# Kernel optimization log

Hardware: AMD Instinct MI355X
Metric: run time of the kernel (lower is better)

## Reference

```python
import jax, jax.numpy as jnp
import numpy as np

# QLSTMClassifier (quantum mode): Embedding -> QLSTM (4 quantum gate layers per step) -> Linear -> log_softmax.
# NOTE: QLSTM.forward unbinds dim 0 (batch) and cats each x:(seq,emb) with hx:(batch,hid),
# which requires batch == seq_len. We honor that with S = batch = seq_len.
S = 256   # batch == seq_len
E = 1024  # embedding_dim
H = 10    # hidden_dim == n_qubits (required by f*cx elementwise product)
V = 50257 # vocab_size
T = 50    # tagset_size


def setup_inputs() -> dict:
    key = jax.random.key(0)
    ks = jax.random.split(key, 6)
    sentence = jax.random.randint(ks[0], (S, S), 0, V)                                   # (batch, seq)
    emb_table = jax.random.normal(ks[1], (V, E), jnp.float32) * 0.02                      # nn.Embedding weight
    Wg = jax.random.normal(ks[2], (4, E + H, H), jnp.float32) * (1.0 / np.sqrt(E + H))    # forget/input/update/output linears
    bg = jnp.zeros((4, H), jnp.float32)
    theta = jax.random.normal(ks[3], (4, H), jnp.float32)                                 # trainable RX angles per gate
    W_out = jax.random.normal(ks[4], (H, T), jnp.float32) * (1.0 / np.sqrt(H))            # hidden2tag
    b_out = jnp.zeros((T,), jnp.float32)
    return dict(sentence=sentence, emb_table=emb_table, Wg=Wg, bg=bg,
                theta=theta, W_out=W_out, b_out=b_out)


def _qlayer(z, th):
    # Exact closed form of the QLayer circuit on n wires starting from |0...0>:
    #   RX(z_w) then RX(th_w) on wire w  ==> RX(a_w) with a_w = z_w + th_w (product state),
    #   then CNOT ring: CNOT(0,1), CNOT(1,2), ..., CNOT(n-2,n-1), CNOT(n-1,0),
    # Heisenberg-picture pullback of Z_w through the CNOT ring gives
    #   M_0 = Z_1 Z_2 ... Z_{n-1},   M_w = Z_0 Z_1 ... Z_w  (w >= 1),
    # and on the product state <Z_j> = cos(a_j), so expectations factorize:
    #   out_0 = prod_{j>=1} cos(a_j),  out_w = prod_{j<=w} cos(a_j).
    c = jnp.cos(z + th)                                   # (B, H)
    cum = jnp.cumprod(c, axis=-1)                         # prefix products
    tail = jnp.prod(c[:, 1:], axis=-1, keepdims=True)     # wire-0 observable
    return jnp.concatenate([tail, cum[:, 1:]], axis=-1)   # (B, H)


def reference(sentence, emb_table, Wg, bg, theta, W_out, b_out):
    embeds = emb_table[sentence]                          # (S, S, E); scan axis = dim 0 (unbind dim)
    h0 = jnp.zeros((embeds.shape[0], theta.shape[1]), embeds.dtype)

    def step(carry, x):                                   # x: (S, E)
        hx, cx = carry
        comb = jnp.concatenate([x, hx], axis=-1)          # (S, E+H)
        z = jnp.einsum('bi,gio->gbo', comb, Wg) + bg[:, None, :]  # (4, S, H)
        f = jax.nn.sigmoid(_qlayer(z[0], theta[0]))
        i = jax.nn.sigmoid(_qlayer(z[1], theta[1]))
        g = jnp.tanh(_qlayer(z[2], theta[2]))
        o = jax.nn.sigmoid(_qlayer(z[3], theta[3]))
        cx = f * cx + i * g
        hx = o * jnp.tanh(cx)
        return (hx, cx), hx

    _, outs = jax.lax.scan(step, (h0, h0), embeds)        # (S, S, H)
    logits = outs @ W_out + b_out                         # (S, S, T)
    return jax.nn.log_softmax(logits, axis=2)
```

## Files before the change

### kernel.cpp

```cpp
#include <hip/hip_runtime.h>
#include <hip/hip_bf16.h>


#define E_DIM 1024
#define H_DIM 10
#define NC 40
#define EHS 10340

typedef __attribute__((ext_vector_type(8))) short bf16x8;
typedef __attribute__((ext_vector_type(4))) float f32x4;

__device__ __forceinline__ unsigned short f2bf(float f) {
    unsigned u = __float_as_uint(f);
    unsigned r = u + 0x7FFFu + ((u >> 16) & 1u);
    return (unsigned short)(r >> 16);
}

__global__ __launch_bounds__(256) void k_wt(const float* __restrict__ Wg,
                                            unsigned short* __restrict__ Bfg) {
    int i = blockIdx.x * 256 + threadIdx.x;
    if (i >= 6144) return;
    int lane = i & 63, nt = (i >> 6) % 3, c = i / 192;
    int kg = lane >> 4, n = lane & 15;
    int nc = nt * 16 + n;
    unsigned short v[8];
#pragma unroll
    for (int j = 0; j < 8; ++j) {
        int k = c * 32 + kg * 8 + j;
        float w = 0.0f;
        if (nc < NC) {
            int g = nc / H_DIM, h = nc % H_DIM;
            w = Wg[g * EHS + k * H_DIM + h];
        }
        v[j] = f2bf(w);
    }
    bf16x8* dst = (bf16x8*)(Bfg + (size_t)i * 8);
    bf16x8 pk;
#pragma unroll
    for (int j = 0; j < 8; ++j) pk[j] = (short)v[j];
    *dst = pk;
}

__global__ __launch_bounds__(256, 4) void k_gemm(const int* __restrict__ idx,
                                                 const float* __restrict__ emb,
                                                 const unsigned short* __restrict__ Bfg,
                                                 float* __restrict__ zs) {
    const int tid = threadIdx.x;
    const int wave = tid >> 6, lane = tid & 63;
    const int R0 = (blockIdx.x * 4 + wave) * 16;
    const int m = lane & 15, q = lane >> 4;

    const int token = idx[R0 + m];
    const float* arow = emb + (size_t)token * E_DIM + q * 8;

    f32x4 acc0 = {0.f, 0.f, 0.f, 0.f}, acc1 = acc0, acc2 = acc0;

#pragma unroll 2
    for (int c = 0; c < 32; ++c) {
        float4 a0 = *(const float4*)(arow + c * 32);
        float4 a1 = *(const float4*)(arow + c * 32 + 4);
        bf16x8 b0 = *(const bf16x8*)(Bfg + ((size_t)(c * 3 + 0) * 64 + lane) * 8);
        bf16x8 b1 = *(const bf16x8*)(Bfg + ((size_t)(c * 3 + 1) * 64 + lane) * 8);
        bf16x8 b2 = *(const bf16x8*)(Bfg + ((size_t)(c * 3 + 2) * 64 + lane) * 8);
        bf16x8 af;
        af[0] = (short)f2bf(a0.x); af[1] = (short)f2bf(a0.y);
        af[2] = (short)f2bf(a0.z); af[3] = (short)f2bf(a0.w);
        af[4] = (short)f2bf(a1.x); af[5] = (short)f2bf(a1.y);
        af[6] = (short)f2bf(a1.z); af[7] = (short)f2bf(a1.w);
        acc0 = __builtin_amdgcn_mfma_f32_16x16x32_bf16(af, b0, acc0, 0, 0, 0);
        acc1 = __builtin_amdgcn_mfma_f32_16x16x32_bf16(af, b1, acc1, 0, 0, 0);
        acc2 = __builtin_amdgcn_mfma_f32_16x16x32_bf16(af, b2, acc2, 0, 0, 0);
    }

    const int t = R0 >> 8;
    const int bbase = (R0 & 255) + q * 4;
#pragma unroll
    for (int i = 0; i < 4; ++i) {
        int b = bbase + i;
        size_t o = ((size_t)b * 256 + t) * NC;
        zs[o + m] = acc0[i];
        zs[o + 16 + m] = acc1[i];
        if (m < 8) zs[o + 32 + m] = acc2[i];
    }
}

template <int CTRL>
__device__ __forceinline__ float dpp1(float x) {
    return __int_as_float(__builtin_amdgcn_update_dpp(
        __float_as_int(1.0f), __float_as_int(x), CTRL, 0xF, 0xF, false));
}
#define ROW_SHR(n) (0x110 + (n))
#define ROW_SHL(n) (0x100 + (n))

__device__ __forceinline__ float rdlane(float v, int l) {
    return __int_as_float(__builtin_amdgcn_readlane(__float_as_int(v), l));
}

__global__ __launch_bounds__(128) void k_rnn(const float* __restrict__ zs,
                                             const float* __restrict__ Wg,
                                             const float* __restrict__ bg,
                                             const float* __restrict__ theta,
                                             float* __restrict__ outs) {
    __shared__ float zbuf[2][640];
    const int tid = threadIdx.x;
    const int b = blockIdx.x;

    if (tid >= 64) {
        const int p = tid - 64;
        const float* src = zs + (size_t)b * 256 * NC;
#pragma unroll
        for (int k = 0; k < 10; ++k) zbuf[0][p + k * 64] = src[p + k * 64];
        __syncthreads();
        for (int blk = 0; blk < 16; ++blk) {
            if (blk + 1 < 16) {
                const float* s2 = src + (blk + 1) * 640;
                float v[10];
#pragma unroll
                for (int k = 0; k < 10; ++k) v[k] = s2[p + k * 64];
#pragma unroll
                for (int k = 0; k < 10; ++k) zbuf[(blk + 1) & 1][p + k * 64] = v[k];
            }
            __syncthreads();
        }
    } else {
        const int lane = tid;
        const int r = lane >> 4;
        const int h = lane & 15;
        const int hc = (h < 10) ? h : 9;
        const int cidx = r * 10 + hc;

        float Wh[10];
#pragma unroll
        for (int j = 0; j < 10; ++j) Wh[j] = Wg[r * EHS + (E_DIM + j) * H_DIM + hc];
        const float bias = bg[cidx] + theta[cidx];

        const float kk = (r == 2) ? 2.0f : -1.0f;
        const float aa = (r == 2) ? 1.0f : 0.0f;
        const float bb = (r == 2) ? -2.0f : 1.0f;

        float cx = 0.0f, hx = 0.0f;
        __syncthreads();

        for (int blk = 0; blk < 16; ++blk) {
            const float* zb = zbuf[blk & 1];
            float zv = zb[cidx];
#pragma unroll 4
            for (int s = 0; s < 16; ++s) {
                float znext = zb[((s < 15) ? (s + 1) * 40 : s * 40) + cidx];

                float hv0 = rdlane(hx, 0), hv1 = rdlane(hx, 1), hv2 = rdlane(hx, 2),
                      hv3 = rdlane(hx, 3), hv4 = rdlane(hx, 4), hv5 = rdlane(hx, 5),
                      hv6 = rdlane(hx, 6), hv7 = rdlane(hx, 7), hv8 = rdlane(hx, 8),
                      hv9 = rdlane(hx, 9);
                float d0 = fmaf(hv0, Wh[0], fmaf(hv2, Wh[2],
                           fmaf(hv4, Wh[4], fmaf(hv6, Wh[6], hv8 * Wh[8]))));
                float d1 = fmaf(hv1, Wh[1], fmaf(hv3, Wh[3],
                           fmaf(hv5, Wh[5], fmaf(hv7, Wh[7], hv9 * Wh[9]))));
                float z = (zv + bias) + (d0 + d1);

                float cc = __builtin_amdgcn_cosf(z * 0.15915494309189535f);

                float pp = cc;
                pp *= dpp1<ROW_SHR(1)>(pp);
                pp *= dpp1<ROW_SHR(2)>(pp);
                pp *= dpp1<ROW_SHR(4)>(pp);
                pp *= dpp1<ROW_SHR(8)>(pp);
                float ss = (h < 10) ? cc : 1.0f;
                ss *= dpp1<ROW_SHL(1)>(ss);
                ss *= dpp1<ROW_SHL(2)>(ss);
                ss *= dpp1<ROW_SHL(4)>(ss);
                ss *= dpp1<ROW_SHL(8)>(ss);
                float tl = dpp1<ROW_SHL(1)>(ss);
                float qv = (h == 0) ? tl : pp;

                float e = __expf(kk * qv);
                float act = fmaf(bb, __builtin_amdgcn_rcpf(1.0f + e), aa);

                float fv = __shfl(act, h);
                float iv = __shfl(act, 16 + h);
                float gv = __shfl(act, 32 + h);
                float ov = __shfl(act, 48 + h);

                cx = fmaf(fv, cx, iv * gv);
                float e2 = __expf(2.0f * cx);
                float th = fmaf(-2.0f, __builtin_amdgcn_rcpf(1.0f + e2), 1.0f);
                hx = ov * th;

                int t = blk * 16 + s;
                if (lane < 10) outs[((size_t)t * 256 + b) * H_DIM + lane] = hx;
                zv = znext;
            }
            __syncthreads();
        }
    }
}

__global__ __launch_bounds__(256) void k_head(const float* __restrict__ outs,
                                              const float* __restrict__ Wo,
                                              const float* __restrict__ bo,
                                              float* __restrict__ out) {
    const size_t row = blockIdx.x * 256 + threadIdx.x;
    float hx[10];
#pragma unroll
    for (int i = 0; i < 5; ++i) {
        float2 v = *(const float2*)&outs[row * H_DIM + 2 * i];
        hx[2 * i] = v.x; hx[2 * i + 1] = v.y;
    }
    float lg[50];
#pragma unroll
    for (int cI = 0; cI < 50; ++cI) {
        float l = bo[cI];
#pragma unroll
        for (int j = 0; j < 10; ++j) l = fmaf(hx[j], Wo[j * 50 + cI], l);
        lg[cI] = l;
    }
    float m = lg[0];
#pragma unroll
    for (int cI = 1; cI < 50; ++cI) m = fmaxf(m, lg[cI]);
    float sum = 0.0f;
#pragma unroll
    for (int cI = 0; cI < 50; ++cI) sum += __expf(lg[cI] - m);
    float lse = m + __logf(sum);
#pragma unroll
    for (int i = 0; i < 25; ++i) {
        float2 v = {lg[2 * i] - lse, lg[2 * i + 1] - lse};
        *(float2*)&out[row * 50 + 2 * i] = v;
    }
}

extern "C" void kernel_launch(void* const* d_in, const int* in_sizes, int n_in,
                              void* d_out, int out_size, void* d_ws, size_t ws_size,
                              hipStream_t stream) {
    const int*   sentence = (const int*)d_in[0];
    const float* emb      = (const float*)d_in[1];
    const float* Wg       = (const float*)d_in[2];
    const float* bg       = (const float*)d_in[3];
    const float* theta    = (const float*)d_in[4];
    const float* Wo       = (const float*)d_in[5];
    const float* bo       = (const float*)d_in[6];
    float* out = (float*)d_out;

    float* ws = (float*)d_ws;
    unsigned short* Bfg = (unsigned short*)ws;
    float* zs   = ws + 24576;
    float* outs = zs + (size_t)256 * 256 * NC;

    k_wt<<<24, 256, 0, stream>>>(Wg, Bfg);
    k_gemm<<<1024, 256, 0, stream>>>(sentence, emb, Bfg, zs);
    k_rnn<<<256, 128, 0, stream>>>(zs, Wg, bg, theta, outs);
    k_head<<<256, 256, 0, stream>>>(outs, Wo, bo, out);
}
```

Measured before the change: 381.5 us.

## Stage embedding rows into LDS via async global_load_lds with double buffering

The gather GEMM no longer reads embedding rows straight from global memory into registers. Each wave now streams its 16 gathered rows into a per-wave double-buffered LDS region with global_load_lds, in 256-float chunks, and hand-placed vmcnt waits let the next chunk load while MFMAs run on the current one. B fragments for eight k-steps are also loaded into registers ahead of use. The cost is 130KB of LDS per block, which forces one block per CU and lowers occupancy, and correctness now depends on the hard-coded vmcnt counts.

Result: no change. 385.6 us (+1.1%).

```diff
diff --git a/kernel.cpp b/kernel.cpp
--- a/kernel.cpp
+++ b/kernel.cpp
@@ -41,35 +41,82 @@
     *dst = pk;
 }
 
-__global__ __launch_bounds__(256, 4) void k_gemm(const int* __restrict__ idx,
+#define CH_F 256
+#define ROWB 1040
+#define WBUF (16 * ROWB)
+#define WAVE_LDS (2 * WBUF)
+
+typedef const __attribute__((address_space(1))) void* gas1_t;
+typedef __attribute__((address_space(3))) void* las3_t;
+
+__device__ __forceinline__ void gload_lds16(const void* g, void* l) {
+    __builtin_amdgcn_global_load_lds((gas1_t)(unsigned long long)g,
+                                     (las3_t)(unsigned)(unsigned long long)l,
+                                     16, 0, 0);
+}
+
+__global__ __launch_bounds__(256, 1) void k_gemm(const int* __restrict__ idx,
                                                  const float* __restrict__ emb,
                                                  const unsigned short* __restrict__ Bfg,
                                                  float* __restrict__ zs) {
+    __shared__ char smem[4 * WAVE_LDS];
     const int tid = threadIdx.x;
     const int wave = tid >> 6, lane = tid & 63;
-    const int R0 = (blockIdx.x * 4 + wave) * 16;
+    const int R0 = blockIdx.x * 64 + wave * 16;
     const int m = lane & 15, q = lane >> 4;
 
-    const int token = idx[R0 + m];
-    const float* arow = emb + (size_t)token * E_DIM + q * 8;
+    char* mybuf = smem + wave * WAVE_LDS;
+
+    const int tok = idx[R0 + m];
+    const float* grow[16];
+#pragma unroll
+    for (int j = 0; j < 16; ++j) {
+        int tj = __builtin_amdgcn_readlane(tok, j);
+        grow[j] = emb + (size_t)tj * E_DIM;
+    }
 
     f32x4 acc0 = {0.f, 0.f, 0.f, 0.f}, acc1 = acc0, acc2 = acc0;
 
-#pragma unroll 2
-    for (int c = 0; c < 32; ++c) {
-        float4 a0 = *(const float4*)(arow + c * 32);
-        float4 a1 = *(const float4*)(arow + c * 32 + 4);
-        bf16x8 b0 = *(const bf16x8*)(Bfg + ((size_t)(c * 3 + 0) * 64 + lane) * 8);
-        bf16x8 b1 = *(const bf16x8*)(Bfg + ((size_t)(c * 3 + 1) * 64 + lane) * 8);
-        bf16x8 b2 = *(const bf16x8*)(Bfg + ((size_t)(c * 3 + 2) * 64 + lane) * 8);
-        bf16x8 af;
-        af[0] = (short)f2bf(a0.x); af[1] = (short)f2bf(a0.y);
-        af[2] = (short)f2bf(a0.z); af[3] = (short)f2bf(a0.w);
-        af[4] = (short)f2bf(a1.x); af[5] = (short)f2bf(a1.y);
-        af[6] = (short)f2bf(a1.z); af[7] = (short)f2bf(a1.w);
-        acc0 = __builtin_amdgcn_mfma_f32_16x16x32_bf16(af, b0, acc0, 0, 0, 0);
-        acc1 = __builtin_amdgcn_mfma_f32_16x16x32_bf16(af, b1, acc1, 0, 0, 0);
-        acc2 = __builtin_amdgcn_mfma_f32_16x16x32_bf16(af, b2, acc2, 0, 0, 0);
+#pragma unroll
+    for (int j = 0; j < 16; ++j)
+        gload_lds16(grow[j] + lane * 4, mybuf + j * ROWB);
+
+#pragma unroll
+    for (int cc = 0; cc < 4; ++cc) {
+        bf16x8 Bv0[8], Bv1[8], Bv2[8];
+#pragma unroll
+        for (int c = 0; c < 8; ++c) {
+            int cg = cc * 8 + c;
+            Bv0[c] = *(const bf16x8*)(Bfg + ((size_t)(cg * 3 + 0) * 64 + lane) * 8);
+            Bv1[c] = *(const bf16x8*)(Bfg + ((size_t)(cg * 3 + 1) * 64 + lane) * 8);
+            Bv2[c] = *(const bf16x8*)(Bfg + ((size_t)(cg * 3 + 2) * 64 + lane) * 8);
+        }
+        asm volatile("" ::: "memory");
+
+        if (cc < 3) {
+#pragma unroll
+            for (int j = 0; j < 16; ++j)
+                gload_lds16(grow[j] + (size_t)(cc + 1) * CH_F + lane * 4,
+                            mybuf + ((cc + 1) & 1) * WBUF + j * ROWB);
+            asm volatile("s_waitcnt vmcnt(40)" ::: "memory");
+        } else {
+            asm volatile("s_waitcnt vmcnt(24)" ::: "memory");
+        }
+
+        const float* ap = (const float*)(mybuf + (cc & 1) * WBUF + m * ROWB);
+#pragma unroll
+        for (int c = 0; c < 8; ++c) {
+            float4 a0 = *(const float4*)(ap + c * 32 + q * 8);
+            float4 a1 = *(const float4*)(ap + c * 32 + q * 8 + 4);
+            bf16x8 af;
+            af[0] = (short)f2bf(a0.x); af[1] = (short)f2bf(a0.y);
+            af[2] = (short)f2bf(a0.z); af[3] = (short)f2bf(a0.w);
+            af[4] = (short)f2bf(a1.x); af[5] = (short)f2bf(a1.y);
+            af[6] = (short)f2bf(a1.z); af[7] = (short)f2bf(a1.w);
+            acc0 = __builtin_amdgcn_mfma_f32_16x16x32_bf16(af, Bv0[c], acc0, 0, 0, 0);
+            acc1 = __builtin_amdgcn_mfma_f32_16x16x32_bf16(af, Bv1[c], acc1, 0, 0, 0);
+            acc2 = __builtin_amdgcn_mfma_f32_16x16x32_bf16(af, Bv2[c], acc2, 0, 0, 0);
+        }
     }
 
     const int t = R0 >> 8;
```

## Project entire vocabulary once, then gather projected gate rows per token

Applied to the files above, without the earlier changes.

The embedding gather and gate projection are reordered. The GEMM now multiplies every vocabulary row of the embedding table by the gate weights, with contiguous row reads, giving a 50257x40 table. The recurrent kernel then gathers 40-float rows from that table by token index. This cuts GEMM rows from 65536 to 50257 and replaces random 4KB embedding reads with sequential streaming, at the cost of small random 160-byte gathers in the RNN loader.

Result: slower. 400.1 us (+4.9%).

```diff
diff --git a/kernel.cpp b/kernel.cpp
--- a/kernel.cpp
+++ b/kernel.cpp
@@ -5,6 +5,7 @@
 #define E_DIM 1024
 #define H_DIM 10
 #define NC 40
+#define V_DIM 50257
 #define EHS 10340
 
 typedef __attribute__((ext_vector_type(8))) short bf16x8;
@@ -41,17 +42,17 @@
     *dst = pk;
 }
 
-__global__ __launch_bounds__(256, 4) void k_gemm(const int* __restrict__ idx,
-                                                 const float* __restrict__ emb,
+__global__ __launch_bounds__(256, 4) void k_gemm(const float* __restrict__ emb,
                                                  const unsigned short* __restrict__ Bfg,
-                                                 float* __restrict__ zs) {
+                                                 float* __restrict__ zu) {
     const int tid = threadIdx.x;
     const int wave = tid >> 6, lane = tid & 63;
     const int R0 = (blockIdx.x * 4 + wave) * 16;
     const int m = lane & 15, q = lane >> 4;
 
-    const int token = idx[R0 + m];
-    const float* arow = emb + (size_t)token * E_DIM + q * 8;
+    int row = R0 + m;
+    if (row > V_DIM - 1) row = V_DIM - 1;
+    const float* arow = emb + (size_t)row * E_DIM + q * 8;
 
     f32x4 acc0 = {0.f, 0.f, 0.f, 0.f}, acc1 = acc0, acc2 = acc0;
 
@@ -72,15 +73,16 @@
         acc2 = __builtin_amdgcn_mfma_f32_16x16x32_bf16(af, b2, acc2, 0, 0, 0);
     }
 
-    const int t = R0 >> 8;
-    const int bbase = (R0 & 255) + q * 4;
+    const int r0 = R0 + q * 4;
 #pragma unroll
     for (int i = 0; i < 4; ++i) {
-        int b = bbase + i;
-        size_t o = ((size_t)b * 256 + t) * NC;
-        zs[o + m] = acc0[i];
-        zs[o + 16 + m] = acc1[i];
-        if (m < 8) zs[o + 32 + m] = acc2[i];
+        int r = r0 + i;
+        if (r < V_DIM) {
+            size_t o = (size_t)r * NC;
+            zu[o + m] = acc0[i];
+            zu[o + 16 + m] = acc1[i];
+            if (m < 8) zu[o + 32 + m] = acc2[i];
+        }
     }
 }
 
@@ -96,29 +98,48 @@
     return __int_as_float(__builtin_amdgcn_readlane(__float_as_int(v), l));
 }
 
-__global__ __launch_bounds__(128) void k_rnn(const float* __restrict__ zs,
+__global__ __launch_bounds__(128) void k_rnn(const int* __restrict__ idx,
+                                             const float* __restrict__ zu,
                                              const float* __restrict__ Wg,
                                              const float* __restrict__ bg,
                                              const float* __restrict__ theta,
                                              float* __restrict__ outs) {
     __shared__ float zbuf[2][640];
+    __shared__ int toks[256];
     const int tid = threadIdx.x;
     const int b = blockIdx.x;
 
     if (tid >= 64) {
         const int p = tid - 64;
-        const float* src = zs + (size_t)b * 256 * NC;
-#pragma unroll
-        for (int k = 0; k < 10; ++k) zbuf[0][p + k * 64] = src[p + k * 64];
+#pragma unroll
+        for (int k = 0; k < 4; ++k) toks[p + k * 64] = idx[(p + k * 64) * 256 + b];
+        const int j = p >> 2;
+        const int s4 = p & 3;
+        {
+            int tv = toks[j];
+            const float* src = zu + (size_t)tv * NC + s4 * 10;
+            float* dst = &zbuf[0][j * 40 + s4 * 10];
+#pragma unroll
+            for (int e = 0; e < 5; ++e)
+                *(float2*)(dst + 2 * e) = *(const float2*)(src + 2 * e);
+        }
         __syncthreads();
         for (int blk = 0; blk < 16; ++blk) {
             if (blk + 1 < 16) {
-                const float* s2 = src + (blk + 1) * 640;
+                int tv = toks[(blk + 1) * 16 + j];
+                const float* src = zu + (size_t)tv * NC + s4 * 10;
                 float v[10];
 #pragma unroll
-                for (int k = 0; k < 10; ++k) v[k] = s2[p + k * 64];
-#pragma unroll
-                for (int k = 0; k < 10; ++k) zbuf[(blk + 1) & 1][p + k * 64] = v[k];
+                for (int e = 0; e < 5; ++e) {
+                    float2 t2 = *(const float2*)(src + 2 * e);
+                    v[2 * e] = t2.x; v[2 * e + 1] = t2.y;
+                }
+                float* dst = &zbuf[(blk + 1) & 1][j * 40 + s4 * 10];
+#pragma unroll
+                for (int e = 0; e < 5; ++e) {
+                    float2 t2 = {v[2 * e], v[2 * e + 1]};
+                    *(float2*)(dst + 2 * e) = t2;
+                }
             }
             __syncthreads();
         }
@@ -242,11 +263,11 @@
 
     float* ws = (float*)d_ws;
     unsigned short* Bfg = (unsigned short*)ws;
-    float* zs   = ws + 24576;
-    float* outs = zs + (size_t)256 * 256 * NC;
+    float* zu   = ws + 24576;
+    float* outs = zu + (size_t)V_DIM * NC;
 
     k_wt<<<24, 256, 0, stream>>>(Wg, Bfg);
-    k_gemm<<<1024, 256, 0, stream>>>(sentence, emb, Bfg, zs);
-    k_rnn<<<256, 128, 0, stream>>>(zs, Wg, bg, theta, outs);
+    k_gemm<<<786, 256, 0, stream>>>(emb, Bfg, zu);
+    k_rnn<<<256, 128, 0, stream>>>(sentence, zu, Wg, bg, theta, outs);
     k_head<<<256, 256, 0, stream>>>(outs, Wo, bo, out);
 }
```
